# Optimization experiments

Measured on AMD Instinct MI355X. Metric: run time of the kernel, lower is better.

## Reference

```python
import jax, jax.numpy as jnp
import numpy as np

NX, NY, NZ = 200, 200, 6          # grid_size
NUM_VOXELS = NX * NY * NZ          # 240000
B, N, C, H, W = 4, 6, 64, 64, 176  # features (B, N_cam, C, H, W)


def setup_inputs() -> dict:
    key = jax.random.key(0)
    k1, k2, k3, k4, k5 = jax.random.split(key, 5)
    feat = jax.random.normal(k1, (B, N, C, H, W), dtype=jnp.float32)
    cam_idx = jax.random.randint(k2, (NUM_VOXELS,), 0, N)
    u_idx = jax.random.randint(k3, (NUM_VOXELS,), 0, W)
    v_idx = jax.random.randint(k4, (NUM_VOXELS,), 0, H)
    valid = jax.random.randint(k5, (NUM_VOXELS,), 0, 2).astype(jnp.bool_)
    return {"feat": feat, "cam_idx": cam_idx, "u_idx": u_idx,
            "v_idx": v_idx, "valid": valid}


def reference(feat, cam_idx, u_idx, v_idx, valid):
    # LUT gather: flat index into per-batch flattened camera features
    flat_idx = cam_idx * (H * W) + v_idx * W + u_idx        # (V,)
    safe_idx = jnp.where(valid, flat_idx, 0)                 # in-range dummy for invalid
    # (B, N, C, H, W) -> (B, N*H*W, C), matching permute(0,1,3,4,2).reshape
    feat_flat = jnp.transpose(feat, (0, 1, 3, 4, 2)).reshape(B, N * H * W, C)
    selected = feat_flat[:, safe_idx, :]                     # (B, V, C)
    # invalid voxels stay zero (scatter into zero tensor in the original)
    out = jnp.where(valid[None, :, None], selected, jnp.zeros((), feat.dtype))
    # (B, V, C) -> (B, nx, ny, nz, C) -> (B, C, nx, ny, nz)
    out = out.reshape(B, NX, NY, NZ, C)
    return jnp.transpose(out, (0, 4, 1, 2, 3))
```

## Files before the change

kernel.cpp:

```cpp
#include <hip/hip_runtime.h>


constexpr int NB   = 4;
constexpr int NCAM = 6;
constexpr int NC   = 64;
constexpr int NH   = 64;
constexpr int NW   = 176;
constexpr int NVOX = 240000;
constexpr int HW   = NH * NW;
constexpr int CHW  = NC * HW;
constexpr int NPIX = NCAM * HW;

constexpr int TILES_B   = NVOX / 64;
constexpr int HALF      = TILES_B / 2;
constexpr int GBLOCKS   = NB * TILES_B;

constexpr size_t WS_NEEDED = (size_t)NB * NPIX * NC * 2;

typedef float        f32x4 __attribute__((ext_vector_type(4)));
typedef unsigned int u32x4 __attribute__((ext_vector_type(4)));

__device__ __forceinline__ unsigned short f32_to_bf16_rne(float f) {
    unsigned int u = __float_as_uint(f);
    u += 0x7FFFu + ((u >> 16) & 1u);
    return (unsigned short)(u >> 16);
}

__global__ __launch_bounds__(256) void transpose_kernel(
    const float* __restrict__ feat, unsigned short* __restrict__ wst)
{
    __shared__ unsigned short lds[64][66];
    const int bid  = blockIdx.x;
    const int tile = bid % (HW / 64);
    const int bn   = bid / (HW / 64);
    const int px0  = tile * 64;
    const int t    = threadIdx.x;

    const float* src = feat + (size_t)bn * CHW + px0;
#pragma unroll
    for (int r = 0; r < 16; ++r) {
        const int c  = r * 4 + (t >> 6);
        const int px = t & 63;
        const float f = __builtin_nontemporal_load(&src[(size_t)c * HW + px]);
        lds[px][c] = f32_to_bf16_rne(f);
    }
    __syncthreads();

    unsigned short* dst = wst + ((size_t)bn * HW + px0) * NC;
#pragma unroll
    for (int j = 0; j < 2; ++j) {
        const int px    = t >> 2;
        const int chunk = (t & 3) + 4 * j;
        u32x4 o;
#pragma unroll
        for (int p = 0; p < 4; ++p) {
            const unsigned int lo = lds[px][chunk * 8 + 2 * p];
            const unsigned int hi = lds[px][chunk * 8 + 2 * p + 1];
            o[p] = lo | (hi << 16);
        }
        *reinterpret_cast<u32x4*>(dst + (size_t)px * NC + chunk * 8) = o;
    }
}

__global__ __launch_bounds__(256) void gather_cl_kernel(
    const unsigned short* __restrict__ wst,
    const int* __restrict__ cam, const int* __restrict__ uu,
    const int* __restrict__ vv,  const int* __restrict__ valid,
    float* __restrict__ out)
{
    __shared__ float ot[64][65];
    __shared__ int   po_s[64];

    const int xcd  = blockIdx.x & 7;
    const int j    = blockIdx.x >> 3;
    const int b    = xcd >> 1;
    const int tile = (xcd & 1) * HALF + j;
    const int vox0 = tile * 64;
    const int t    = threadIdx.x;

    if (t < 64) {
        const int i = vox0 + t;
        po_s[t] = valid[i] ? cam[i] * HW + vv[i] * NW + uu[i] : -1;
    }
    __syncthreads();

    const unsigned short* wb = wst + (size_t)b * NPIX * NC;
#pragma unroll
    for (int r = 0; r < 2; ++r) {
        const int vox = r * 32 + (t >> 3);
        const int k   = t & 7;
        const int pix = po_s[vox];
        if (pix >= 0) {
            const u32x4 raw = *reinterpret_cast<const u32x4*>(
                wb + (size_t)pix * NC + k * 8);
#pragma unroll
            for (int p = 0; p < 4; ++p) {
                ot[k * 8 + 2 * p][vox]     = __uint_as_float(raw[p] << 16);
                ot[k * 8 + 2 * p + 1][vox] = __uint_as_float(raw[p] & 0xFFFF0000u);
            }
        } else {
#pragma unroll
            for (int e = 0; e < 8; ++e) ot[k * 8 + e][vox] = 0.0f;
        }
    }
    __syncthreads();

    float* ob = out + (size_t)b * NC * NVOX + vox0;
#pragma unroll
    for (int i = 0; i < 4; ++i) {
        const int slot = i * 256 + t;
        const int ch   = slot >> 4;
        const int g    = slot & 15;
        f32x4 val = { ot[ch][4 * g], ot[ch][4 * g + 1],
                      ot[ch][4 * g + 2], ot[ch][4 * g + 3] };
        __builtin_nontemporal_store(val,
            reinterpret_cast<f32x4*>(ob + (size_t)ch * NVOX + 4 * g));
    }
}

__global__ __launch_bounds__(256) void gather_direct_kernel(
    const float* __restrict__ feat,
    const int* __restrict__ cam, const int* __restrict__ u,
    const int* __restrict__ v,   const int* __restrict__ valid,
    float* __restrict__ out)
{
    const int NG = NVOX / 4;
    const int t  = blockIdx.x * 256 + threadIdx.x;
    const int g  = t % NG;
    const int bc = t / NG;
    const int c  = bc & (NC - 1);
    const int b  = bc >> 6;
    const int4 c4 = reinterpret_cast<const int4*>(cam)[g];
    const int4 u4 = reinterpret_cast<const int4*>(u)[g];
    const int4 v4 = reinterpret_cast<const int4*>(v)[g];
    const int4 w4 = reinterpret_cast<const int4*>(valid)[g];
    const float* fb = feat + (size_t)b * (NCAM * CHW) + (size_t)c * HW;
    float4 o;
    o.x = w4.x ? fb[c4.x * CHW + v4.x * NW + u4.x] : 0.0f;
    o.y = w4.y ? fb[c4.y * CHW + v4.y * NW + u4.y] : 0.0f;
    o.z = w4.z ? fb[c4.z * CHW + v4.z * NW + u4.z] : 0.0f;
    o.w = w4.w ? fb[c4.w * CHW + v4.w * NW + u4.w] : 0.0f;
    reinterpret_cast<float4*>(out)[t] = o;
}

extern "C" void kernel_launch(void* const* d_in, const int* in_sizes, int n_in,
                              void* d_out, int out_size, void* d_ws, size_t ws_size,
                              hipStream_t stream) {
    const float* feat  = (const float*)d_in[0];
    const int*   cam   = (const int*)d_in[1];
    const int*   u     = (const int*)d_in[2];
    const int*   v     = (const int*)d_in[3];
    const int*   valid = (const int*)d_in[4];
    float* out = (float*)d_out;

    if (ws_size >= WS_NEEDED) {
        unsigned short* wst = (unsigned short*)d_ws;
        transpose_kernel<<<NB * NCAM * (HW / 64), 256, 0, stream>>>(feat, wst);
        gather_cl_kernel<<<GBLOCKS, 256, 0, stream>>>(wst, cam, u, v, valid, out);
    } else {
        const int total = NB * NC * (NVOX / 4);
        gather_direct_kernel<<<total / 256, 256, 0, stream>>>(feat, cam, u, v, valid, out);
    }
}
```

Before: 74.01 us.

## Process two batches per gather block to reuse LUT indices across batches

Each gather block now handles one voxel tile for two batches in turn, reusing the computed pixel offsets, and the block count is halved. The XCD mapping is reworked so each XCD covers a batch pair and a quarter of the tiles, with an early exit for tail blocks. This saves repeated index loads and offset math, but each block does more serial work with an extra barrier, and the per-XCD L2 now holds two batches' workspace slices.

```diff
diff --git a/kernel.cpp b/kernel.cpp
--- a/kernel.cpp
+++ b/kernel.cpp
@@ -11,9 +11,9 @@
 constexpr int CHW  = NC * HW;
 constexpr int NPIX = NCAM * HW;
 
-constexpr int TILES_B   = NVOX / 64;
-constexpr int HALF      = TILES_B / 2;
-constexpr int GBLOCKS   = NB * TILES_B;
+constexpr int TILES_B  = NVOX / 64;
+constexpr int KPX      = (TILES_B + 3) / 4;
+constexpr int GBLOCKS  = 8 * KPX;
 
 constexpr size_t WS_NEEDED = (size_t)NB * NPIX * NC * 2;
 
@@ -72,9 +72,11 @@
     __shared__ int   po_s[64];
 
     const int xcd  = blockIdx.x & 7;
-    const int j    = blockIdx.x >> 3;
-    const int b    = xcd >> 1;
-    const int tile = (xcd & 1) * HALF + j;
+    const int bp   = xcd >> 2;
+    const int q    = xcd & 3;
+    const int k    = blockIdx.x >> 3;
+    const int tile = q * KPX + k;
+    if (tile >= TILES_B) return;
     const int vox0 = tile * 64;
     const int t    = threadIdx.x;
 
@@ -84,38 +86,46 @@
     }
     __syncthreads();
 
-    const unsigned short* wb = wst + (size_t)b * NPIX * NC;
+    const int vox = (t >> 3) & 31;
 #pragma unroll
-    for (int r = 0; r < 2; ++r) {
-        const int vox = r * 32 + (t >> 3);
-        const int k   = t & 7;
-        const int pix = po_s[vox];
-        if (pix >= 0) {
-            const u32x4 raw = *reinterpret_cast<const u32x4*>(
-                wb + (size_t)pix * NC + k * 8);
+    for (int bb = 0; bb < 2; ++bb) {
+        const int b = 2 * bp + bb;
+        const unsigned short* wb = wst + (size_t)b * NPIX * NC;
+
 #pragma unroll
-            for (int p = 0; p < 4; ++p) {
-                ot[k * 8 + 2 * p][vox]     = __uint_as_float(raw[p] << 16);
-                ot[k * 8 + 2 * p + 1][vox] = __uint_as_float(raw[p] & 0xFFFF0000u);
+        for (int r = 0; r < 2; ++r) {
+            const int vx  = r * 32 + (t >> 3);
+            const int kk  = t & 7;
+            const int pix = po_s[vx];
+            if (pix >= 0) {
+                const u32x4 raw = *reinterpret_cast<const u32x4*>(
+                    wb + (size_t)pix * NC + kk * 8);
+#pragma unroll
+                for (int p = 0; p < 4; ++p) {
+                    ot[kk * 8 + 2 * p][vx]     = __uint_as_float(raw[p] << 16);
+                    ot[kk * 8 + 2 * p + 1][vx] = __uint_as_float(raw[p] & 0xFFFF0000u);
+                }
+            } else {
+#pragma unroll
+                for (int e = 0; e < 8; ++e) ot[kk * 8 + e][vx] = 0.0f;
             }
-        } else {
+        }
+        __syncthreads();
+
+        float* ob = out + (size_t)b * NC * NVOX + vox0;
 #pragma unroll
-            for (int e = 0; e < 8; ++e) ot[k * 8 + e][vox] = 0.0f;
+        for (int i = 0; i < 4; ++i) {
+            const int slot = i * 256 + t;
+            const int ch   = slot >> 4;
+            const int g    = slot & 15;
+            f32x4 val = { ot[ch][4 * g], ot[ch][4 * g + 1],
+                          ot[ch][4 * g + 2], ot[ch][4 * g + 3] };
+            __builtin_nontemporal_store(val,
+                reinterpret_cast<f32x4*>(ob + (size_t)ch * NVOX + 4 * g));
         }
+        if (bb == 0) __syncthreads();
     }
-    __syncthreads();
-
-    float* ob = out + (size_t)b * NC * NVOX + vox0;
-#pragma unroll
-    for (int i = 0; i < 4; ++i) {
-        const int slot = i * 256 + t;
-        const int ch   = slot >> 4;
-        const int g    = slot & 15;
-        f32x4 val = { ot[ch][4 * g], ot[ch][4 * g + 1],
-                      ot[ch][4 * g + 2], ot[ch][4 * g + 3] };
-        __builtin_nontemporal_store(val,
-            reinterpret_cast<f32x4*>(ob + (size_t)ch * NVOX + 4 * g));
-    }
+    (void)vox;
 }
 
 __global__ __launch_bounds__(256) void gather_direct_kernel(
```

Result: no change. 74.11 us (+0.1%).
